# Performance work log

Measured on AMD Instinct MI355X. Metric: run time of the kernel, lower is better.

## Reference

```python
import jax, jax.numpy as jnp
import numpy as np

B, N, NIN, NH, NOUT = 32, 64, 256, 256, 2
E = N * (N - 1)
BN_EPS = 1e-5


def _xavier(k, fan_in, fan_out):
    return jax.random.normal(k, (fan_in, fan_out), jnp.float32) * np.sqrt(2.0 / (fan_in + fan_out))


def _mlp_params(key, n_in, n_hid, n_out):
    k1, k2 = jax.random.split(key)
    return {
        'w1': _xavier(k1, n_in, n_hid), 'b1': jnp.full((n_hid,), 0.1, jnp.float32),
        'w2': _xavier(k2, n_hid, n_out), 'b2': jnp.full((n_out,), 0.1, jnp.float32),
        'g': jnp.ones((n_out,), jnp.float32), 'beta': jnp.zeros((n_out,), jnp.float32),
    }


def setup_inputs() -> dict:
    key = jax.random.key(0)
    ks = jax.random.split(key, 7)
    inputs = jax.random.normal(ks[0], (B, N, NIN), jnp.float32)
    # fully-connected directed graph w/o self loops: edge e = (send i, recv j), i != j
    idx = np.array([(i, j) for i in range(N) for j in range(N) if i != j], dtype=np.int64)
    rel_send = np.zeros((E, N), np.float32)
    rel_rec = np.zeros((E, N), np.float32)
    rel_send[np.arange(E), idx[:, 0]] = 1.0
    rel_rec[np.arange(E), idx[:, 1]] = 1.0
    out = {'inputs': inputs, 'rel_rec': jnp.asarray(rel_rec), 'rel_send': jnp.asarray(rel_send)}
    for name, (ni, nh, no), k in [('mlp1', (NIN, NH, NH), ks[1]),
                                  ('mlp2', (2 * NH, NH, NH), ks[2]),
                                  ('mlp3', (NH, NH, NH), ks[3]),
                                  ('mlp4', (3 * NH, NH, NH), ks[4])]:
        p = _mlp_params(k, ni, nh, no)
        for pk, pv in p.items():
            out[f'{name}_{pk}'] = pv
    out['fc_w'] = _xavier(ks[5], NH, NOUT)
    out['fc_b'] = jnp.full((NOUT,), 0.1, jnp.float32)
    return out


def _mlp(x, w1, b1, w2, b2, g, beta):
    # Linear -> ELU -> Linear -> ELU -> BatchNorm1d (training-mode batch stats, biased var)
    h = jax.nn.elu(x @ w1 + b1)
    h = jax.nn.elu(h @ w2 + b2)
    mean = h.mean(axis=(0, 1))
    var = h.var(axis=(0, 1))
    return (h - mean) * jax.lax.rsqrt(var + BN_EPS) * g + beta


def reference(inputs, rel_rec, rel_send,
              mlp1_w1, mlp1_b1, mlp1_w2, mlp1_b2, mlp1_g, mlp1_beta,
              mlp2_w1, mlp2_b1, mlp2_w2, mlp2_b2, mlp2_g, mlp2_beta,
              mlp3_w1, mlp3_b1, mlp3_w2, mlp3_b2, mlp3_g, mlp3_beta,
              mlp4_w1, mlp4_b1, mlp4_w2, mlp4_b2, mlp4_g, mlp4_beta,
              fc_w, fc_b):
    x = _mlp(inputs, mlp1_w1, mlp1_b1, mlp1_w2, mlp1_b2, mlp1_g, mlp1_beta)  # [B,N,NH]
    # node2edge: gather sender/receiver node features per edge
    s = jnp.einsum('en,bnh->beh', rel_send, x)
    r = jnp.einsum('en,bnh->beh', rel_rec, x)
    x = jnp.concatenate([s, r], axis=-1)  # [B,E,2*NH]
    x = _mlp(x, mlp2_w1, mlp2_b1, mlp2_w2, mlp2_b2, mlp2_g, mlp2_beta)
    x_skip = x
    # edge2node: scatter-sum incoming edges per node, normalized by N
    inc = jnp.einsum('en,beh->bnh', rel_rec, x) / N
    x = _mlp(inc, mlp3_w1, mlp3_b1, mlp3_w2, mlp3_b2, mlp3_g, mlp3_beta)
    s = jnp.einsum('en,bnh->beh', rel_send, x)
    r = jnp.einsum('en,bnh->beh', rel_rec, x)
    x = jnp.concatenate([s, r, x_skip], axis=-1)  # [B,E,3*NH]
    x = _mlp(x, mlp4_w1, mlp4_b1, mlp4_w2, mlp4_b2, mlp4_g, mlp4_beta)
    return x @ fc_w + fc_b  # [B,E,NOUT]
```

## Files before the change

kernel.cpp:

```cpp
#include <hip/hip_runtime.h>

typedef __bf16 bf16_t;
typedef __bf16 bf16x8 __attribute__((ext_vector_type(8)));
typedef float  f32x4  __attribute__((ext_vector_type(4)));

#define NB    64
#define EB    4032
#define BATCH 32
#define H     256
#define M_EDGE (BATCH*EB)
#define M_NODE (BATCH*NB)
#define T2    4
#define BN_EPS 1e-5f

__device__ __forceinline__ void load_lds16(const void* g, void* l) {
    __builtin_amdgcn_global_load_lds(
        (const __attribute__((address_space(1))) unsigned int*)g,
        (__attribute__((address_space(3))) unsigned int*)l, 16, 0, 0);
}
__device__ __forceinline__ float elu(float v) { return v > 0.f ? v : __expf(v) - 1.f; }

template<bool AF32>
__global__ __launch_bounds__(256, 3)
void fused_mlp(const void* __restrict__ A0v,
               const bf16_t* __restrict__ W1f, const float* __restrict__ b1,
               const bf16_t* __restrict__ W2f, const float* __restrict__ b2,
               bf16_t* __restrict__ out, float* __restrict__ stats)
{
    const int m0 = blockIdx.x * 64;
    const int tid = threadIdx.x, wave = tid >> 6, lane = tid & 63;
    const int l15 = lane & 15, quad = lane >> 4;
    const int row = tid >> 2;
    const int c0 = (tid & 3) * 64;

    __shared__ bf16_t h1s[64 * 264];
    __shared__ float  sred[512];

    sred[tid] = 0.f; sred[256 + tid] = 0.f;

    if (AF32) {
        const float* af = (const float*)A0v + (size_t)(m0 + row) * 256 + c0;
#pragma unroll
        for (int j = 0; j < 8; ++j) {
            float4 lo = *(const float4*)(af + j * 8);
            float4 hi = *(const float4*)(af + j * 8 + 4);
            bf16x8 v;
            v[0]=(bf16_t)lo.x; v[1]=(bf16_t)lo.y; v[2]=(bf16_t)lo.z; v[3]=(bf16_t)lo.w;
            v[4]=(bf16_t)hi.x; v[5]=(bf16_t)hi.y; v[6]=(bf16_t)hi.z; v[7]=(bf16_t)hi.w;
            *(bf16x8*)&h1s[row * 264 + c0 + j * 8] = v;
        }
    } else {
        const bf16_t* src = (const bf16_t*)A0v + (size_t)(m0 + row) * 256 + c0;
#pragma unroll
        for (int j = 0; j < 8; ++j)
            *(bf16x8*)&h1s[row * 264 + c0 + j * 8] = *(const bf16x8*)(src + j * 8);
    }

    const bf16_t* W1W = W1f + (size_t)wave * 16384;
    const bf16_t* W2W = W2f + (size_t)wave * 16384;

    bf16x8 bcur[4], bnxt[4];
#pragma unroll
    for (int u = 0; u < 4; ++u)
        bcur[u] = *(const bf16x8*)(W1W + u * 512 + lane * 8);
    __syncthreads();

    f32x4 acc[4][4];
#pragma unroll
    for (int a = 0; a < 4; ++a)
#pragma unroll
        for (int u = 0; u < 4; ++u) acc[a][u] = (f32x4){0.f, 0.f, 0.f, 0.f};

#pragma unroll
    for (int ks = 0; ks < 8; ++ks) {
        if (ks < 7) {
#pragma unroll
            for (int u = 0; u < 4; ++u)
                bnxt[u] = *(const bf16x8*)(W1W + (ks + 1) * 2048 + u * 512 + lane * 8);
        }
        bf16x8 afr[4];
#pragma unroll
        for (int a = 0; a < 4; ++a)
            afr[a] = *(const bf16x8*)&h1s[(a * 16 + l15) * 264 + ks * 32 + quad * 8];
#pragma unroll
        for (int a = 0; a < 4; ++a)
#pragma unroll
            for (int u = 0; u < 4; ++u)
                acc[a][u] = __builtin_amdgcn_mfma_f32_16x16x32_bf16(afr[a], bcur[u], acc[a][u], 0, 0, 0);
#pragma unroll
        for (int u = 0; u < 4; ++u) bcur[u] = bnxt[u];
    }

#pragma unroll
    for (int u = 0; u < 4; ++u)
        bcur[u] = *(const bf16x8*)(W2W + u * 512 + lane * 8);
    __syncthreads();

#pragma unroll
    for (int u = 0; u < 4; ++u) {
        int   col = wave * 64 + u * 16 + l15;
        float bv  = b1[col];
#pragma unroll
        for (int a = 0; a < 4; ++a)
#pragma unroll
            for (int r = 0; r < 4; ++r)
                h1s[(a * 16 + quad * 4 + r) * 264 + col] = (bf16_t)elu(acc[a][u][r] + bv);
    }
    __syncthreads();

#pragma unroll
    for (int a = 0; a < 4; ++a)
#pragma unroll
        for (int u = 0; u < 4; ++u) acc[a][u] = (f32x4){0.f, 0.f, 0.f, 0.f};
#pragma unroll
    for (int ks = 0; ks < 8; ++ks) {
        if (ks < 7) {
#pragma unroll
            for (int u = 0; u < 4; ++u)
                bnxt[u] = *(const bf16x8*)(W2W + (ks + 1) * 2048 + u * 512 + lane * 8);
        }
        bf16x8 afr[4];
#pragma unroll
        for (int a = 0; a < 4; ++a)
            afr[a] = *(const bf16x8*)&h1s[(a * 16 + l15) * 264 + ks * 32 + quad * 8];
#pragma unroll
        for (int a = 0; a < 4; ++a)
#pragma unroll
            for (int u = 0; u < 4; ++u)
                acc[a][u] = __builtin_amdgcn_mfma_f32_16x16x32_bf16(afr[a], bcur[u], acc[a][u], 0, 0, 0);
#pragma unroll
        for (int u = 0; u < 4; ++u) bcur[u] = bnxt[u];
    }
    __syncthreads();

#pragma unroll
    for (int u = 0; u < 4; ++u) {
        int   col = wave * 64 + u * 16 + l15;
        float bv  = b2[col];
        float s = 0.f, q = 0.f;
#pragma unroll
        for (int a = 0; a < 4; ++a)
#pragma unroll
            for (int r = 0; r < 4; ++r) {
                float v = elu(acc[a][u][r] + bv);
                h1s[(a * 16 + quad * 4 + r) * 264 + col] = (bf16_t)v;
                s += v; q += v * v;
            }
        s += __shfl_xor(s, 16); s += __shfl_xor(s, 32);
        q += __shfl_xor(q, 16); q += __shfl_xor(q, 32);
        if (quad == 0) { atomicAdd(&sred[col], s); atomicAdd(&sred[256 + col], q); }
    }
    __syncthreads();

#pragma unroll
    for (int p = 0; p < 8; ++p) {
        int idx = p * 256 + tid;
        int r = idx >> 5, ch = idx & 31;
        *(uint4*)&out[(size_t)(m0 + r) * H + ch * 8] = *(const uint4*)&h1s[r * 264 + ch * 8];
    }
    atomicAdd(&stats[tid],     sred[tid]);
    atomicAdd(&stats[H + tid], sred[256 + tid]);
}

__global__ __launch_bounds__(256)
void node_gemm(const bf16_t* __restrict__ A, const float* __restrict__ statsIn,
               const float* __restrict__ g, const float* __restrict__ beta, float Mcnt,
               const bf16_t* __restrict__ Wt, const float* __restrict__ bias,
               float* __restrict__ out)
{
    const int m0 = blockIdx.x * 64;
    const int nb = blockIdx.y * 256;
    const int tid = threadIdx.x, wave = tid >> 6, lane = tid & 63;
    const int l15 = lane & 15, quad = lane >> 4;
    const int row = tid >> 2;
    const int cx8 = (((tid & 3) ^ ((tid >> 3) & 3))) * 8;
    const int sl8 = (tid & 3) * 8;
    const int xq8 = (quad ^ ((l15 >> 1) & 3)) * 8;
    __shared__ bf16_t As[64 * 32];
    __shared__ bf16_t Bs[256 * 32];
    __shared__ float  ss[512];

    {
        float mean = statsIn[tid] / Mcnt;
        float var  = statsIn[256 + tid] / Mcnt - mean * mean;
        float scl  = g[tid] * rsqrtf(var + BN_EPS);
        ss[tid]       = scl;
        ss[256 + tid] = beta[tid] - mean * scl;
    }
    __syncthreads();

    f32x4 acc[4][4];
#pragma unroll
    for (int t = 0; t < 4; ++t)
#pragma unroll
        for (int u = 0; u < 4; ++u) acc[t][u] = (f32x4){0.f, 0.f, 0.f, 0.f};

    for (int k0 = 0; k0 < 256; k0 += 32) {
        {
            int kc = k0 + cx8;
            bf16x8 v = *(const bf16x8*)(A + (size_t)(m0 + row) * 256 + kc);
            bf16x8 w;
#pragma unroll
            for (int j = 0; j < 8; ++j)
                w[j] = (bf16_t)((float)v[j] * ss[kc + j] + ss[256 + kc + j]);
            *(bf16x8*)&As[row * 32 + sl8] = w;
        }
#pragma unroll
        for (int p = 0; p < 4; ++p)
            load_lds16(Wt + (size_t)(nb + p * 64 + row) * 256 + k0 + cx8,
                       Bs + (p * 256 + wave * 64) * 8);
        __syncthreads();
        bf16x8 afr[4], bfr[4];
#pragma unroll
        for (int t = 0; t < 4; ++t)
            afr[t] = *(const bf16x8*)&As[(t * 16 + l15) * 32 + xq8];
#pragma unroll
        for (int u = 0; u < 4; ++u)
            bfr[u] = *(const bf16x8*)&Bs[(wave * 64 + u * 16 + l15) * 32 + xq8];
#pragma unroll
        for (int t = 0; t < 4; ++t)
#pragma unroll
            for (int u = 0; u < 4; ++u)
                acc[t][u] = __builtin_amdgcn_mfma_f32_16x16x32_bf16(afr[t], bfr[u], acc[t][u], 0, 0, 0);
        __syncthreads();
    }
#pragma unroll
    for (int u = 0; u < 4; ++u) {
        int col = nb + wave * 64 + u * 16 + l15;
        float bv = bias[col];
#pragma unroll
        for (int t = 0; t < 4; ++t)
#pragma unroll
            for (int r = 0; r < 4; ++r)
                out[(size_t)(m0 + t * 16 + quad * 4 + r) * 512 + col] = acc[t][u][r] + bv;
    }
}

__global__ __launch_bounds__(256, 2)
void m2_kernel(const float* __restrict__ PQ, const bf16_t* __restrict__ W2t,
               const float* __restrict__ b2, bf16_t* __restrict__ out,
               float* __restrict__ stats)
{
    const int tile0 = blockIdx.x * T2;
    const int tid = threadIdx.x, wave = tid >> 6, lane = tid & 63;
    const int l15 = lane & 15, quad = lane >> 4;

    __shared__ bf16_t Abuf[2][64 * 264];
    __shared__ float  sred[512];

    bf16x8 Breg[32];
#pragma unroll
    for (int ks = 0; ks < 8; ++ks)
#pragma unroll
        for (int u = 0; u < 4; ++u) {
            int col = wave * 64 + u * 16 + l15;
            Breg[ks * 4 + u] = *(const bf16x8*)(W2t + (size_t)col * 256 + ks * 32 + quad * 8);
        }
    sred[tid] = 0.f; sred[256 + tid] = 0.f;

    auto computeA = [&](int t, int b) {
        int row = tid >> 2;
        int m = (tile0 + t) * 64 + row;
        int bb = m / EB, e = m - bb * EB;
        int sn = e / (NB - 1), rr = e - sn * (NB - 1);
        int rc = rr + (rr >= sn ? 1 : 0);
        const float* Prow = PQ + (size_t)(bb * NB + sn) * 512;
        const float* Qrow = PQ + (size_t)(bb * NB + rc) * 512 + 256;
        int c0 = (tid & 3) * 64;
#pragma unroll
        for (int j = 0; j < 8; ++j) {
            int c = c0 + j * 8;
            float4 p0 = *(const float4*)(Prow + c);
            float4 p1 = *(const float4*)(Prow + c + 4);
            float4 q0 = *(const float4*)(Qrow + c);
            float4 q1 = *(const float4*)(Qrow + c + 4);
            bf16x8 v;
            v[0]=(bf16_t)elu(p0.x+q0.x); v[1]=(bf16_t)elu(p0.y+q0.y);
            v[2]=(bf16_t)elu(p0.z+q0.z); v[3]=(bf16_t)elu(p0.w+q0.w);
            v[4]=(bf16_t)elu(p1.x+q1.x); v[5]=(bf16_t)elu(p1.y+q1.y);
            v[6]=(bf16_t)elu(p1.z+q1.z); v[7]=(bf16_t)elu(p1.w+q1.w);
            *(bf16x8*)&Abuf[b][row * 264 + c] = v;
        }
    };

    computeA(0, 0);
    __syncthreads();

    for (int t = 0; t < T2; ++t) {
        const int cur = t & 1, nxt = cur ^ 1;
        if (t + 1 < T2) computeA(t + 1, nxt);

        f32x4 acc[4][4];
#pragma unroll
        for (int a = 0; a < 4; ++a)
#pragma unroll
            for (int u = 0; u < 4; ++u) acc[a][u] = (f32x4){0.f, 0.f, 0.f, 0.f};
#pragma unroll
        for (int ks = 0; ks < 8; ++ks) {
            bf16x8 afr[4];
#pragma unroll
            for (int a = 0; a < 4; ++a)
                afr[a] = *(const bf16x8*)&Abuf[cur][(a * 16 + l15) * 264 + ks * 32 + quad * 8];
#pragma unroll
            for (int a = 0; a < 4; ++a)
#pragma unroll
                for (int u = 0; u < 4; ++u)
                    acc[a][u] = __builtin_amdgcn_mfma_f32_16x16x32_bf16(afr[a], Breg[ks * 4 + u], acc[a][u], 0, 0, 0);
        }
        __syncthreads();

#pragma unroll
        for (int u = 0; u < 4; ++u) {
            int   col = wave * 64 + u * 16 + l15;
            float bv  = b2[col];
            float s = 0.f, q = 0.f;
#pragma unroll
            for (int a = 0; a < 4; ++a)
#pragma unroll
                for (int r = 0; r < 4; ++r) {
                    float v = elu(acc[a][u][r] + bv);
                    Abuf[cur][(a * 16 + quad * 4 + r) * 264 + col] = (bf16_t)v;
                    s += v; q += v * v;
                }
            s += __shfl_xor(s, 16); s += __shfl_xor(s, 32);
            q += __shfl_xor(q, 16); q += __shfl_xor(q, 32);
            if (quad == 0) { atomicAdd(&sred[col], s); atomicAdd(&sred[256 + col], q); }
        }
        __syncthreads();

        size_t m0 = (size_t)(tile0 + t) * 64;
#pragma unroll
        for (int p = 0; p < 8; ++p) {
            int idx = p * 256 + tid;
            int r = idx >> 5, ch = idx & 31;
            *(uint4*)&out[(m0 + r) * H + ch * 8] = *(const uint4*)&Abuf[cur][r * 264 + ch * 8];
        }
        __syncthreads();
    }
    atomicAdd(&stats[tid],     sred[tid]);
    atomicAdd(&stats[H + tid], sred[256 + tid]);
}

__global__ __launch_bounds__(256, 3)
void m4_kernel(const bf16_t* __restrict__ h2, const bf16_t* __restrict__ Wskf,
               const float* __restrict__ RS, const bf16_t* __restrict__ W4f,
               const float* __restrict__ b2, bf16_t* __restrict__ out,
               float* __restrict__ stats)
{
    const int m0 = blockIdx.x * 64;
    const int tid = threadIdx.x, wave = tid >> 6, lane = tid & 63;
    const int l15 = lane & 15, quad = lane >> 4;
    const int row = tid >> 2;
    const int cx8 = (((tid & 3) ^ ((tid >> 3) & 3))) * 8;
    const int xq8 = (quad ^ ((l15 >> 1) & 3)) * 8;

    __shared__ bf16_t h1s[8 * 2048];
    __shared__ float  sred[512];

    sred[tid] = 0.f; sred[256 + tid] = 0.f;

    const int bb  = m0 / EB;
    const int e0  = m0 - bb * EB;
    const int sn0 = e0 / (NB - 1);
    const int rr0 = e0 - sn0 * (NB - 1);
    const float* RSb = RS + (size_t)(bb * NB) * 512;

#pragma unroll
    for (int ks = 0; ks < 8; ++ks)
        load_lds16(h2 + (size_t)(m0 + row) * 256 + ks * 32 + cx8,
                   h1s + ks * 2048 + wave * 512);

    f32x4 acc[4][4];
#pragma unroll
    for (int a = 0; a < 4; ++a)
#pragma unroll
        for (int r = 0; r < 4; ++r) {
            int ro = a * 16 + quad * 4 + r;
            int t  = rr0 + ro;
            int wrap = (t >= NB - 1) ? 1 : 0;
            int sn = sn0 + wrap;
            int rr = t - (wrap ? (NB - 1) : 0);
            int rc = rr + (rr >= sn ? 1 : 0);
            const float* Srow = RSb + (size_t)sn * 512;
            const float* Rrow = RSb + (size_t)rc * 512 + 256;
#pragma unroll
            for (int u = 0; u < 4; ++u) {
                int co = wave * 64 + u * 16 + l15;
                acc[a][u][r] = Srow[co] + Rrow[co];
            }
        }

    const bf16_t* WskW = Wskf + (size_t)wave * 16384;
    const bf16_t* W4W  = W4f  + (size_t)wave * 16384;

    bf16x8 bcur[4], bnxt[4];
#pragma unroll
    for (int u = 0; u < 4; ++u)
        bcur[u] = *(const bf16x8*)(WskW + u * 512 + lane * 8);
    __syncthreads();

#pragma unroll
    for (int ks = 0; ks < 8; ++ks) {
        if (ks < 7) {
#pragma unroll
            for (int u = 0; u < 4; ++u)
                bnxt[u] = *(const bf16x8*)(WskW + (ks + 1) * 2048 + u * 512 + lane * 8);
        }
        bf16x8 afr[4];
#pragma unroll
        for (int a = 0; a < 4; ++a)
            afr[a] = *(const bf16x8*)&h1s[ks * 2048 + (a * 16 + l15) * 32 + xq8];
#pragma unroll
        for (int a = 0; a < 4; ++a)
#pragma unroll
            for (int u = 0; u < 4; ++u)
                acc[a][u] = __builtin_amdgcn_mfma_f32_16x16x32_bf16(afr[a], bcur[u], acc[a][u], 0, 0, 0);
#pragma unroll
        for (int u = 0; u < 4; ++u) bcur[u] = bnxt[u];
    }

#pragma unroll
    for (int u = 0; u < 4; ++u)
        bcur[u] = *(const bf16x8*)(W4W + u * 512 + lane * 8);
    __syncthreads();

#pragma unroll
    for (int u = 0; u < 4; ++u) {
        const int ks = wave * 2 + (u >> 1);
        const int qw = (u & 1) * 2 + (l15 >> 3);
        const int j  = l15 & 7;
#pragma unroll
        for (int a = 0; a < 4; ++a)
#pragma unroll
            for (int r = 0; r < 4; ++r) {
                int rw = a * 16 + quad * 4 + r;
                int qp = qw ^ ((rw >> 1) & 3);
                h1s[ks * 2048 + rw * 32 + qp * 8 + j] = (bf16_t)elu(acc[a][u][r]);
            }
    }
    __syncthreads();

#pragma unroll
    for (int a = 0; a < 4; ++a)
#pragma unroll
        for (int u = 0; u < 4; ++u) acc[a][u] = (f32x4){0.f, 0.f, 0.f, 0.f};
#pragma unroll
    for (int ks = 0; ks < 8; ++ks) {
        if (ks < 7) {
#pragma unroll
            for (int u = 0; u < 4; ++u)
                bnxt[u] = *(const bf16x8*)(W4W + (ks + 1) * 2048 + u * 512 + lane * 8);
        }
        bf16x8 afr[4];
#pragma unroll
        for (int a = 0; a < 4; ++a)
            afr[a] = *(const bf16x8*)&h1s[ks * 2048 + (a * 16 + l15) * 32 + xq8];
#pragma unroll
        for (int a = 0; a < 4; ++a)
#pragma unroll
            for (int u = 0; u < 4; ++u)
                acc[a][u] = __builtin_amdgcn_mfma_f32_16x16x32_bf16(afr[a], bcur[u], acc[a][u], 0, 0, 0);
#pragma unroll
        for (int u = 0; u < 4; ++u) bcur[u] = bnxt[u];
    }
    __syncthreads();

#pragma unroll
    for (int u = 0; u < 4; ++u) {
        const int col = wave * 64 + u * 16 + l15;
        const float bv = b2[col];
        const int ks = wave * 2 + (u >> 1);
        const int qw = (u & 1) * 2 + (l15 >> 3);
        const int j  = l15 & 7;
        float s = 0.f, q = 0.f;
#pragma unroll
        for (int a = 0; a < 4; ++a)
#pragma unroll
            for (int r = 0; r < 4; ++r) {
                float v = elu(acc[a][u][r] + bv);
                int rw = a * 16 + quad * 4 + r;
                int qp = qw ^ ((rw >> 1) & 3);
                h1s[ks * 2048 + rw * 32 + qp * 8 + j] = (bf16_t)v;
                s += v; q += v * v;
            }
        s += __shfl_xor(s, 16); s += __shfl_xor(s, 32);
        q += __shfl_xor(q, 16); q += __shfl_xor(q, 32);
        if (quad == 0) { atomicAdd(&sred[col], s); atomicAdd(&sred[256 + col], q); }
    }
    __syncthreads();

#pragma unroll
    for (int p = 0; p < 8; ++p) {
        int idx = p * 256 + tid;
        int r = idx >> 5, ch = idx & 31;
        *(uint4*)&out[(size_t)(m0 + r) * H + ch * 8] =
            *(const uint4*)&h1s[(ch >> 2) * 2048 + r * 32 + (((ch & 3) ^ ((r >> 1) & 3)) * 8)];
    }
    atomicAdd(&stats[tid],     sred[tid]);
    atomicAdd(&stats[H + tid], sred[256 + tid]);
}

__global__ void prep(const float* __restrict__ w1a, bf16_t* __restrict__ wt1a,
                     const float* __restrict__ w1b, bf16_t* __restrict__ wt1b,
                     const float* __restrict__ w2b, bf16_t* __restrict__ wt2b,
                     const float* __restrict__ w3a, bf16_t* __restrict__ wt3a,
                     const float* __restrict__ w3b, bf16_t* __restrict__ wt3b,
                     const float* __restrict__ w4b, bf16_t* __restrict__ wt4b,
                     const float* __restrict__ w2a, bf16_t* __restrict__ wtpq,
                     const float* __restrict__ w4a, bf16_t* __restrict__ wtrs,
                     const float* __restrict__ b2a, float* __restrict__ biasPQ,
                     float* __restrict__ stats)
{
    int blk = blockIdx.x, tid = threadIdx.x;
    if (blk < 1536) {
        int grp = blk >> 8, lb = blk & 255;
        int idx = lb * 256 + tid;
        int k = idx >> 8, n = idx & 255;
        if (grp == 2) {
            wt2b[n * 256 + k] = (bf16_t)w2b[idx];
        } else {
            const float* w; bf16_t* wt;
            switch (grp) {
                case 0: w = w1a; wt = wt1a; break;
                case 1: w = w1b; wt = wt1b; break;
                case 3: w = w3a; wt = wt3a; break;
                case 4: w = w3b; wt = wt3b; break;
                default: w = w4b; wt = wt4b; break;
            }
            int wv = n >> 6, u = (n >> 4) & 3, l15 = n & 15;
            int ks = k >> 5, qd = (k >> 3) & 3, j = k & 7;
            wt[wv * 16384 + ks * 2048 + u * 512 + (qd * 16 + l15) * 8 + j] = (bf16_t)w[idx];
        }
    } else if (blk < 2560) {
        int lb = blk - 1536;
        const float* w = (lb < 512) ? w2a : w4a;
        bf16_t* wt = (lb < 512) ? wtpq : wtrs;
        int c = lb & 511, k = tid;
        float v = (c < 256) ? w[k * 256 + c] : w[(256 + k) * 256 + (c - 256)];
        wt[c * 256 + k] = (bf16_t)v;
    } else if (blk == 2560) {
        biasPQ[tid] = b2a[tid];
        biasPQ[256 + tid] = 0.f;
    } else {
        for (int j = 0; j < 8; ++j) stats[j * 256 + tid] = 0.f;
    }
}

__global__ void prep2(const float* __restrict__ w4a, const float* __restrict__ stats2,
                      const float* __restrict__ g2, const float* __restrict__ be2,
                      const float* __restrict__ b4a, bf16_t* __restrict__ wt,
                      float* __restrict__ bias)
{
    __shared__ float sh2s[256];
    int blk = blockIdx.x, tid = threadIdx.x;
    float mean = stats2[tid] / (float)M_EDGE;
    float var  = stats2[256 + tid] / (float)M_EDGE - mean * mean;
    float scl  = g2[tid] * rsqrtf(var + BN_EPS);
    if (blk < 256) {
        int n = blk, k = tid;
        int wv = n >> 6, u = (n >> 4) & 3, l15 = n & 15;
        int ks = k >> 5, qd = (k >> 3) & 3, j = k & 7;
        wt[wv * 16384 + ks * 2048 + u * 512 + (qd * 16 + l15) * 8 + j] =
            (bf16_t)(w4a[(512 + tid) * 256 + blk] * scl);
    } else {
        sh2s[tid] = be2[tid] - mean * scl;
        __syncthreads();
        float acc = 0.f;
        for (int k = 0; k < 256; ++k)
            acc += sh2s[k] * w4a[(512 + k) * 256 + tid];
        bias[tid] = b4a[tid] + acc;
        bias[256 + tid] = 0.f;
    }
}

__global__ void edge2node(const bf16_t* __restrict__ x2, const float* __restrict__ stats2,
                          const float* __restrict__ g2, const float* __restrict__ be2,
                          bf16_t* __restrict__ inc)
{
    int bn = blockIdx.x, bb = bn >> 6, n = bn & 63;
    int g = threadIdx.x >> 5, t = threadIdx.x & 31;
    __shared__ float part[8][256];
    __shared__ float ss[512];
    {
        int c = threadIdx.x;
        float mean = stats2[c] / (float)M_EDGE;
        float var  = stats2[256 + c] / (float)M_EDGE - mean * mean;
        float scl  = g2[c] * rsqrtf(var + BN_EPS);
        ss[c]       = scl;
        ss[256 + c] = be2[c] - mean * scl;
    }
    const bf16_t* base = x2 + (size_t)bb * EB * H;
    float a[8] = {0.f,0.f,0.f,0.f,0.f,0.f,0.f,0.f};
    for (int i = g; i < NB; i += 8) {
        if (i == n) continue;
        int e = i * (NB - 1) + n - (n > i ? 1 : 0);
        bf16x8 v = *(const bf16x8*)&base[(size_t)e * H + t * 8];
#pragma unroll
        for (int j = 0; j < 8; ++j) a[j] += (float)v[j];
    }
#pragma unroll
    for (int j = 0; j < 8; ++j) part[g][t * 8 + j] = a[j];
    __syncthreads();
    int c = threadIdx.x;
    float s = 0.f;
#pragma unroll
    for (int g2i = 0; g2i < 8; ++g2i) s += part[g2i][c];
    inc[(size_t)bn * H + c] = (bf16_t)(s * (1.f / 64.f) * ss[c] + ss[256 + c] * (63.f / 64.f));
}

__global__ void fc_kernel(const bf16_t* __restrict__ x4, const float* __restrict__ stats4,
                          const float* __restrict__ g4, const float* __restrict__ be4,
                          const float* __restrict__ fcw, const float* __restrict__ fcb,
                          float* __restrict__ out)
{
    __shared__ float ss[512];
    {
        int c = threadIdx.x;
        float mean = stats4[c] / (float)M_EDGE;
        float var  = stats4[256 + c] / (float)M_EDGE - mean * mean;
        float scl  = g4[c] * rsqrtf(var + BN_EPS);
        ss[c]       = scl;
        ss[256 + c] = be4[c] - mean * scl;
    }
    __syncthreads();
    int row  = blockIdx.x * 8 + (threadIdx.x >> 5);
    int t    = threadIdx.x & 31;
    bf16x8 v8 = *(const bf16x8*)(x4 + (size_t)row * H + t * 8);
    float s0 = 0.f, s1 = 0.f;
#pragma unroll
    for (int j = 0; j < 8; ++j) {
        int c = t * 8 + j;
        float v = (float)v8[j] * ss[c] + ss[256 + c];
        s0 += v * fcw[c * 2];
        s1 += v * fcw[c * 2 + 1];
    }
#pragma unroll
    for (int off = 16; off; off >>= 1) {
        s0 += __shfl_down(s0, off, 32);
        s1 += __shfl_down(s1, off, 32);
    }
    if (t == 0) {
        out[(size_t)row * 2]     = s0 + fcb[0];
        out[(size_t)row * 2 + 1] = s1 + fcb[1];
    }
}

extern "C" void kernel_launch(void* const* d_in, const int* in_sizes, int n_in,
                              void* d_out, int out_size, void* d_ws, size_t ws_size,
                              hipStream_t stream)
{
    (void)in_sizes; (void)n_in; (void)out_size; (void)ws_size;
    const float* inp = (const float*)d_in[0];
    const float* w1a = (const float*)d_in[3];  const float* b1a = (const float*)d_in[4];
    const float* w1b = (const float*)d_in[5];  const float* b1b = (const float*)d_in[6];
    const float* g1  = (const float*)d_in[7];  const float* be1 = (const float*)d_in[8];
    const float* w2a = (const float*)d_in[9];  const float* b2a = (const float*)d_in[10];
    const float* w2b = (const float*)d_in[11]; const float* b2b = (const float*)d_in[12];
    const float* g2  = (const float*)d_in[13]; const float* be2 = (const float*)d_in[14];
    const float* w3a = (const float*)d_in[15]; const float* b3a = (const float*)d_in[16];
    const float* w3b = (const float*)d_in[17]; const float* b3b = (const float*)d_in[18];
    const float* g3  = (const float*)d_in[19]; const float* be3 = (const float*)d_in[20];
    const float* w4a = (const float*)d_in[21]; const float* b4a = (const float*)d_in[22];
    const float* w4b = (const float*)d_in[23]; const float* b4b = (const float*)d_in[24];
    const float* g4  = (const float*)d_in[25]; const float* be4 = (const float*)d_in[26];
    const float* fcw = (const float*)d_in[27]; const float* fcb = (const float*)d_in[28];

    char* p = (char*)d_ws;
    auto alloc = [&](size_t nbytes) { char* r = p; p += (nbytes + 255) & ~(size_t)255; return r; };

    bf16_t* wt1a = (bf16_t*)alloc(256 * 256 * 2);
    bf16_t* wt1b = (bf16_t*)alloc(256 * 256 * 2);
    bf16_t* wt2b = (bf16_t*)alloc(256 * 256 * 2);
    bf16_t* wt3a = (bf16_t*)alloc(256 * 256 * 2);
    bf16_t* wt3b = (bf16_t*)alloc(256 * 256 * 2);
    bf16_t* wt4b = (bf16_t*)alloc(256 * 256 * 2);
    bf16_t* wtpq = (bf16_t*)alloc(512 * 256 * 2);
    bf16_t* wtrs = (bf16_t*)alloc(512 * 256 * 2);
    bf16_t* wtsk = (bf16_t*)alloc(256 * 256 * 2);
    float*  biasPQ = (float*)alloc(512 * sizeof(float));
    float*  biasRS = (float*)alloc(512 * sizeof(float));
    float*  stats  = (float*)alloc(4 * 512 * sizeof(float));
    bf16_t* x1   = (bf16_t*)alloc((size_t)M_NODE * H * 2);
    bf16_t* incb = (bf16_t*)alloc((size_t)M_NODE * H * 2);
    bf16_t* x3   = (bf16_t*)alloc((size_t)M_NODE * H * 2);
    float*  PQ   = (float*)alloc((size_t)M_NODE * 512 * sizeof(float));
    float*  RS   = (float*)alloc((size_t)M_NODE * 512 * sizeof(float));
    bf16_t* h2   = (bf16_t*)alloc((size_t)M_EDGE * H * 2);
    bf16_t* h4   = (bf16_t*)alloc((size_t)M_EDGE * H * 2);

    prep<<<2562, 256, 0, stream>>>(w1a, wt1a, w1b, wt1b, w2b, wt2b, w3a, wt3a,
                                   w3b, wt3b, w4b, wt4b, w2a, wtpq, w4a, wtrs,
                                   b2a, biasPQ, stats);

    fused_mlp<true ><<<M_NODE / 64, 256, 0, stream>>>(inp, wt1a, b1a, wt1b, b1b, x1, stats + 0);

    { dim3 g(M_NODE / 64, 2);
      node_gemm<<<g, 256, 0, stream>>>(x1, stats + 0, g1, be1, (float)M_NODE, wtpq, biasPQ, PQ); }

    m2_kernel<<<M_EDGE / (64 * T2), 256, 0, stream>>>(PQ, wt2b, b2b, h2, stats + 512);

    edge2node<<<M_NODE, 256, 0, stream>>>(h2, stats + 512, g2, be2, incb);
    fused_mlp<false><<<M_NODE / 64, 256, 0, stream>>>(incb, wt3a, b3a, wt3b, b3b, x3, stats + 1024);

    prep2<<<257, 256, 0, stream>>>(w4a, stats + 512, g2, be2, b4a, wtsk, biasRS);
    { dim3 g(M_NODE / 64, 2);
      node_gemm<<<g, 256, 0, stream>>>(x3, stats + 1024, g3, be3, (float)M_NODE, wtrs, biasRS, RS); }

    m4_kernel<<<M_EDGE / 64, 256, 0, stream>>>(h2, wtsk, RS, wt4b, b4b, h4, stats + 1536);

    fc_kernel<<<M_EDGE / 8, 256, 0, stream>>>(h4, stats + 1536, g4, be4, fcw, fcb, (float*)d_out);
}
```

Baseline: 352.5 us.

## Restructure m2 kernel to one tile per block with swizzled LDS and streamed weights

The edge-layer second GEMM kernel no longer loops over four 64-row tiles with the whole W2 slice held in registers and a double-buffered A tile. Each block now handles a single 64-row tile. It builds the ELU(P+Q) tile into an XOR-swizzled LDS layout and streams pre-swizzled W2 fragments from global memory per k-step, the same way m4_kernel does. The prep kernel now emits W2 in that fragment layout. This cuts register pressure (occupancy 2 to 3 blocks per CU) and LDS bank conflicts, at the cost of reloading weights per tile and losing the overlap of A computation with the MFMAs.

```diff
diff --git a/kernel.cpp b/kernel.cpp
--- a/kernel.cpp
+++ b/kernel.cpp
@@ -10,7 +10,6 @@
 #define H     256
 #define M_EDGE (BATCH*EB)
 #define M_NODE (BATCH*NB)
-#define T2    4
 #define BN_EPS 1e-5f
 
 __device__ __forceinline__ void load_lds16(const void* g, void* l) {
@@ -236,37 +235,37 @@
     }
 }
 
-__global__ __launch_bounds__(256, 2)
-void m2_kernel(const float* __restrict__ PQ, const bf16_t* __restrict__ W2t,
+__global__ __launch_bounds__(256, 3)
+void m2_kernel(const float* __restrict__ PQ, const bf16_t* __restrict__ W2f,
                const float* __restrict__ b2, bf16_t* __restrict__ out,
                float* __restrict__ stats)
 {
-    const int tile0 = blockIdx.x * T2;
+    const int m0 = blockIdx.x * 64;
     const int tid = threadIdx.x, wave = tid >> 6, lane = tid & 63;
     const int l15 = lane & 15, quad = lane >> 4;
-
-    __shared__ bf16_t Abuf[2][64 * 264];
+    const int row = tid >> 2;
+    const int c0 = (tid & 3) * 64;
+    const int xq8 = (quad ^ ((l15 >> 1) & 3)) * 8;
+
+    __shared__ bf16_t h1s[8 * 2048];
     __shared__ float  sred[512];
 
-    bf16x8 Breg[32];
-#pragma unroll
-    for (int ks = 0; ks < 8; ++ks)
-#pragma unroll
-        for (int u = 0; u < 4; ++u) {
-            int col = wave * 64 + u * 16 + l15;
-            Breg[ks * 4 + u] = *(const bf16x8*)(W2t + (size_t)col * 256 + ks * 32 + quad * 8);
-        }
     sred[tid] = 0.f; sred[256 + tid] = 0.f;
 
-    auto computeA = [&](int t, int b) {
-        int row = tid >> 2;
-        int m = (tile0 + t) * 64 + row;
-        int bb = m / EB, e = m - bb * EB;
-        int sn = e / (NB - 1), rr = e - sn * (NB - 1);
+    const int bb  = m0 / EB;
+    const int e0  = m0 - bb * EB;
+    const int sn0 = e0 / (NB - 1);
+    const int rr0 = e0 - sn0 * (NB - 1);
+
+    {
+        int t  = rr0 + row;
+        int wrap = (t >= NB - 1) ? 1 : 0;
+        int sn = sn0 + wrap;
+        int rr = t - (wrap ? (NB - 1) : 0);
         int rc = rr + (rr >= sn ? 1 : 0);
         const float* Prow = PQ + (size_t)(bb * NB + sn) * 512;
         const float* Qrow = PQ + (size_t)(bb * NB + rc) * 512 + 256;
-        int c0 = (tid & 3) * 64;
+        const int rs = ((row >> 1) & 3);
 #pragma unroll
         for (int j = 0; j < 8; ++j) {
             int c = c0 + j * 8;
@@ -279,177 +278,29 @@
             v[2]=(bf16_t)elu(p0.z+q0.z); v[3]=(bf16_t)elu(p0.w+q0.w);
             v[4]=(bf16_t)elu(p1.x+q1.x); v[5]=(bf16_t)elu(p1.y+q1.y);
             v[6]=(bf16_t)elu(p1.z+q1.z); v[7]=(bf16_t)elu(p1.w+q1.w);
-            *(bf16x8*)&Abuf[b][row * 264 + c] = v;
-        }
-    };
-
-    computeA(0, 0);
-    __syncthreads();
-
-    for (int t = 0; t < T2; ++t) {
-        const int cur = t & 1, nxt = cur ^ 1;
-        if (t + 1 < T2) computeA(t + 1, nxt);
-
-        f32x4 acc[4][4];
-#pragma unroll
-        for (int a = 0; a < 4; ++a)
-#pragma unroll
-            for (int u = 0; u < 4; ++u) acc[a][u] = (f32x4){0.f, 0.f, 0.f, 0.f};
-#pragma unroll
-        for (int ks = 0; ks < 8; ++ks) {
-            bf16x8 afr[4];
-#pragma unroll
-            for (int a = 0; a < 4; ++a)
-                afr[a] = *(const bf16x8*)&Abuf[cur][(a * 16 + l15) * 264 + ks * 32 + quad * 8];
-#pragma unroll
-            for (int a = 0; a < 4; ++a)
-#pragma unroll
-                for (int u = 0; u < 4; ++u)
-                    acc[a][u] = __builtin_amdgcn_mfma_f32_16x16x32_bf16(afr[a], Breg[ks * 4 + u], acc[a][u], 0, 0, 0);
-        }
-        __syncthreads();
-
-#pragma unroll
-        for (int u = 0; u < 4; ++u) {
-            int   col = wave * 64 + u * 16 + l15;
-            float bv  = b2[col];
-            float s = 0.f, q = 0.f;
-#pragma unroll
-            for (int a = 0; a < 4; ++a)
-#pragma unroll
-                for (int r = 0; r < 4; ++r) {
-                    float v = elu(acc[a][u][r] + bv);
-                    Abuf[cur][(a * 16 + quad * 4 + r) * 264 + col] = (bf16_t)v;
-                    s += v; q += v * v;
-                }
-            s += __shfl_xor(s, 16); s += __shfl_xor(s, 32);
-            q += __shfl_xor(q, 16); q += __shfl_xor(q, 32);
-            if (quad == 0) { atomicAdd(&sred[col], s); atomicAdd(&sred[256 + col], q); }
-        }
-        __syncthreads();
-
-        size_t m0 = (size_t)(tile0 + t) * 64;
-#pragma unroll
-        for (int p = 0; p < 8; ++p) {
-            int idx = p * 256 + tid;
-            int r = idx >> 5, ch = idx & 31;
-            *(uint4*)&out[(m0 + r) * H + ch * 8] = *(const uint4*)&Abuf[cur][r * 264 + ch * 8];
-        }
-        __syncthreads();
-    }
-    atomicAdd(&stats[tid],     sred[tid]);
-    atomicAdd(&stats[H + tid], sred[256 + tid]);
-}
-
-__global__ __launch_bounds__(256, 3)
-void m4_kernel(const bf16_t* __restrict__ h2, const bf16_t* __restrict__ Wskf,
-               const float* __restrict__ RS, const bf16_t* __restrict__ W4f,
-               const float* __restrict__ b2, bf16_t* __restrict__ out,
-               float* __restrict__ stats)
-{
-    const int m0 = blockIdx.x * 64;
-    const int tid = threadIdx.x, wave = tid >> 6, lane = tid & 63;
-    const int l15 = lane & 15, quad = lane >> 4;
-    const int row = tid >> 2;
-    const int cx8 = (((tid & 3) ^ ((tid >> 3) & 3))) * 8;
-    const int xq8 = (quad ^ ((l15 >> 1) & 3)) * 8;
-
-    __shared__ bf16_t h1s[8 * 2048];
-    __shared__ float  sred[512];
-
-    sred[tid] = 0.f; sred[256 + tid] = 0.f;
-
-    const int bb  = m0 / EB;
-    const int e0  = m0 - bb * EB;
-    const int sn0 = e0 / (NB - 1);
-    const int rr0 = e0 - sn0 * (NB - 1);
-    const float* RSb = RS + (size_t)(bb * NB) * 512;
-
-#pragma unroll
-    for (int ks = 0; ks < 8; ++ks)
-        load_lds16(h2 + (size_t)(m0 + row) * 256 + ks * 32 + cx8,
-                   h1s + ks * 2048 + wave * 512);
+            *(bf16x8*)&h1s[(c >> 5) * 2048 + row * 32 + ((((c >> 3) & 3) ^ rs) * 8)] = v;
+        }
+    }
+
+    const bf16_t* W2W = W2f + (size_t)wave * 16384;
+    bf16x8 bcur[4], bnxt[4];
+#pragma unroll
+    for (int u = 0; u < 4; ++u)
+        bcur[u] = *(const bf16x8*)(W2W + u * 512 + lane * 8);
+    __syncthreads();
 
     f32x4 acc[4][4];
 #pragma unroll
     for (int a = 0; a < 4; ++a)
 #pragma unroll
-        for (int r = 0; r < 4; ++r) {
-            int ro = a * 16 + quad * 4 + r;
-            int t  = rr0 + ro;
-            int wrap = (t >= NB - 1) ? 1 : 0;
-            int sn = sn0 + wrap;
-            int rr = t - (wrap ? (NB - 1) : 0);
-            int rc = rr + (rr >= sn ? 1 : 0);
-            const float* Srow = RSb + (size_t)sn * 512;
-            const float* Rrow = RSb + (size_t)rc * 512 + 256;
-#pragma unroll
-            for (int u = 0; u < 4; ++u) {
-                int co = wave * 64 + u * 16 + l15;
-                acc[a][u][r] = Srow[co] + Rrow[co];
-            }
-        }
-
-    const bf16_t* WskW = Wskf + (size_t)wave * 16384;
-    const bf16_t* W4W  = W4f  + (size_t)wave * 16384;
-
-    bf16x8 bcur[4], bnxt[4];
-#pragma unroll
-    for (int u = 0; u < 4; ++u)
-        bcur[u] = *(const bf16x8*)(WskW + u * 512 + lane * 8);
-    __syncthreads();
+        for (int u = 0; u < 4; ++u) acc[a][u] = (f32x4){0.f, 0.f, 0.f, 0.f};
 
 #pragma unroll
     for (int ks = 0; ks < 8; ++ks) {
         if (ks < 7) {
 #pragma unroll
             for (int u = 0; u < 4; ++u)
-                bnxt[u] = *(const bf16x8*)(WskW + (ks + 1) * 2048 + u * 512 + lane * 8);
-        }
-        bf16x8 afr[4];
-#pragma unroll
-        for (int a = 0; a < 4; ++a)
-            afr[a] = *(const bf16x8*)&h1s[ks * 2048 + (a * 16 + l15) * 32 + xq8];
-#pragma unroll
-        for (int a = 0; a < 4; ++a)
-#pragma unroll
-            for (int u = 0; u < 4; ++u)
-                acc[a][u] = __builtin_amdgcn_mfma_f32_16x16x32_bf16(afr[a], bcur[u], acc[a][u], 0, 0, 0);
-#pragma unroll
-        for (int u = 0; u < 4; ++u) bcur[u] = bnxt[u];
-    }
-
-#pragma unroll
-    for (int u = 0; u < 4; ++u)
-        bcur[u] = *(const bf16x8*)(W4W + u * 512 + lane * 8);
-    __syncthreads();
-
-#pragma unroll
-    for (int u = 0; u < 4; ++u) {
-        const int ks = wave * 2 + (u >> 1);
-        const int qw = (u & 1) * 2 + (l15 >> 3);
-        const int j  = l15 & 7;
-#pragma unroll
-        for (int a = 0; a < 4; ++a)
-#pragma unroll
-            for (int r = 0; r < 4; ++r) {
-                int rw = a * 16 + quad * 4 + r;
-                int qp = qw ^ ((rw >> 1) & 3);
-                h1s[ks * 2048 + rw * 32 + qp * 8 + j] = (bf16_t)elu(acc[a][u][r]);
-            }
-    }
-    __syncthreads();
-
-#pragma unroll
-    for (int a = 0; a < 4; ++a)
-#pragma unroll
-        for (int u = 0; u < 4; ++u) acc[a][u] = (f32x4){0.f, 0.f, 0.f, 0.f};
-#pragma unroll
-    for (int ks = 0; ks < 8; ++ks) {
-        if (ks < 7) {
-#pragma unroll
-            for (int u = 0; u < 4; ++u)
-                bnxt[u] = *(const bf16x8*)(W4W + (ks + 1) * 2048 + u * 512 + lane * 8);
+                bnxt[u] = *(const bf16x8*)(W2W + (ks + 1) * 2048 + u * 512 + lane * 8);
         }
         bf16x8 afr[4];
 #pragma unroll
@@ -500,6 +351,165 @@
     atomicAdd(&stats[H + tid], sred[256 + tid]);
 }
 
+__global__ __launch_bounds__(256, 3)
+void m4_kernel(const bf16_t* __restrict__ h2, const bf16_t* __restrict__ Wskf,
+               const float* __restrict__ RS, const bf16_t* __restrict__ W4f,
+               const float* __restrict__ b2, bf16_t* __restrict__ out,
+               float* __restrict__ stats)
+{
+    const int m0 = blockIdx.x * 64;
+    const int tid = threadIdx.x, wave = tid >> 6, lane = tid & 63;
+    const int l15 = lane & 15, quad = lane >> 4;
+    const int row = tid >> 2;
+    const int cx8 = (((tid & 3) ^ ((tid >> 3) & 3))) * 8;
+    const int xq8 = (quad ^ ((l15 >> 1) & 3)) * 8;
+
+    __shared__ bf16_t h1s[8 * 2048];
+    __shared__ float  sred[512];
+
+    sred[tid] = 0.f; sred[256 + tid] = 0.f;
+
+    const int bb  = m0 / EB;
+    const int e0  = m0 - bb * EB;
+    const int sn0 = e0 / (NB - 1);
+    const int rr0 = e0 - sn0 * (NB - 1);
+    const float* RSb = RS + (size_t)(bb * NB) * 512;
+
+#pragma unroll
+    for (int ks = 0; ks < 8; ++ks)
+        load_lds16(h2 + (size_t)(m0 + row) * 256 + ks * 32 + cx8,
+                   h1s + ks * 2048 + wave * 512);
+
+    f32x4 acc[4][4];
+#pragma unroll
+    for (int a = 0; a < 4; ++a)
+#pragma unroll
+        for (int r = 0; r < 4; ++r) {
+            int ro = a * 16 + quad * 4 + r;
+            int t  = rr0 + ro;
+            int wrap = (t >= NB - 1) ? 1 : 0;
+            int sn = sn0 + wrap;
+            int rr = t - (wrap ? (NB - 1) : 0);
+            int rc = rr + (rr >= sn ? 1 : 0);
+            const float* Srow = RSb + (size_t)sn * 512;
+            const float* Rrow = RSb + (size_t)rc * 512 + 256;
+#pragma unroll
+            for (int u = 0; u < 4; ++u) {
+                int co = wave * 64 + u * 16 + l15;
+                acc[a][u][r] = Srow[co] + Rrow[co];
+            }
+        }
+
+    const bf16_t* WskW = Wskf + (size_t)wave * 16384;
+    const bf16_t* W4W  = W4f  + (size_t)wave * 16384;
+
+    bf16x8 bcur[4], bnxt[4];
+#pragma unroll
+    for (int u = 0; u < 4; ++u)
+        bcur[u] = *(const bf16x8*)(WskW + u * 512 + lane * 8);
+    __syncthreads();
+
+#pragma unroll
+    for (int ks = 0; ks < 8; ++ks) {
+        if (ks < 7) {
+#pragma unroll
+            for (int u = 0; u < 4; ++u)
+                bnxt[u] = *(const bf16x8*)(WskW + (ks + 1) * 2048 + u * 512 + lane * 8);
+        }
+        bf16x8 afr[4];
+#pragma unroll
+        for (int a = 0; a < 4; ++a)
+            afr[a] = *(const bf16x8*)&h1s[ks * 2048 + (a * 16 + l15) * 32 + xq8];
+#pragma unroll
+        for (int a = 0; a < 4; ++a)
+#pragma unroll
+            for (int u = 0; u < 4; ++u)
+                acc[a][u] = __builtin_amdgcn_mfma_f32_16x16x32_bf16(afr[a], bcur[u], acc[a][u], 0, 0, 0);
+#pragma unroll
+        for (int u = 0; u < 4; ++u) bcur[u] = bnxt[u];
+    }
+
+#pragma unroll
+    for (int u = 0; u < 4; ++u)
+        bcur[u] = *(const bf16x8*)(W4W + u * 512 + lane * 8);
+    __syncthreads();
+
+#pragma unroll
+    for (int u = 0; u < 4; ++u) {
+        const int ks = wave * 2 + (u >> 1);
+        const int qw = (u & 1) * 2 + (l15 >> 3);
+        const int j  = l15 & 7;
+#pragma unroll
+        for (int a = 0; a < 4; ++a)
+#pragma unroll
+            for (int r = 0; r < 4; ++r) {
+                int rw = a * 16 + quad * 4 + r;
+                int qp = qw ^ ((rw >> 1) & 3);
+                h1s[ks * 2048 + rw * 32 + qp * 8 + j] = (bf16_t)elu(acc[a][u][r]);
+            }
+    }
+    __syncthreads();
+
+#pragma unroll
+    for (int a = 0; a < 4; ++a)
+#pragma unroll
+        for (int u = 0; u < 4; ++u) acc[a][u] = (f32x4){0.f, 0.f, 0.f, 0.f};
+#pragma unroll
+    for (int ks = 0; ks < 8; ++ks) {
+        if (ks < 7) {
+#pragma unroll
+            for (int u = 0; u < 4; ++u)
+                bnxt[u] = *(const bf16x8*)(W4W + (ks + 1) * 2048 + u * 512 + lane * 8);
+        }
+        bf16x8 afr[4];
+#pragma unroll
+        for (int a = 0; a < 4; ++a)
+            afr[a] = *(const bf16x8*)&h1s[ks * 2048 + (a * 16 + l15) * 32 + xq8];
+#pragma unroll
+        for (int a = 0; a < 4; ++a)
+#pragma unroll
+            for (int u = 0; u < 4; ++u)
+                acc[a][u] = __builtin_amdgcn_mfma_f32_16x16x32_bf16(afr[a], bcur[u], acc[a][u], 0, 0, 0);
+#pragma unroll
+        for (int u = 0; u < 4; ++u) bcur[u] = bnxt[u];
+    }
+    __syncthreads();
+
+#pragma unroll
+    for (int u = 0; u < 4; ++u) {
+        const int col = wave * 64 + u * 16 + l15;
+        const float bv = b2[col];
+        const int ks = wave * 2 + (u >> 1);
+        const int qw = (u & 1) * 2 + (l15 >> 3);
+        const int j  = l15 & 7;
+        float s = 0.f, q = 0.f;
+#pragma unroll
+        for (int a = 0; a < 4; ++a)
+#pragma unroll
+            for (int r = 0; r < 4; ++r) {
+                float v = elu(acc[a][u][r] + bv);
+                int rw = a * 16 + quad * 4 + r;
+                int qp = qw ^ ((rw >> 1) & 3);
+                h1s[ks * 2048 + rw * 32 + qp * 8 + j] = (bf16_t)v;
+                s += v; q += v * v;
+            }
+        s += __shfl_xor(s, 16); s += __shfl_xor(s, 32);
+        q += __shfl_xor(q, 16); q += __shfl_xor(q, 32);
+        if (quad == 0) { atomicAdd(&sred[col], s); atomicAdd(&sred[256 + col], q); }
+    }
+    __syncthreads();
+
+#pragma unroll
+    for (int p = 0; p < 8; ++p) {
+        int idx = p * 256 + tid;
+        int r = idx >> 5, ch = idx & 31;
+        *(uint4*)&out[(size_t)(m0 + r) * H + ch * 8] =
+            *(const uint4*)&h1s[(ch >> 2) * 2048 + r * 32 + (((ch & 3) ^ ((r >> 1) & 3)) * 8)];
+    }
+    atomicAdd(&stats[tid],     sred[tid]);
+    atomicAdd(&stats[H + tid], sred[256 + tid]);
+}
+
 __global__ void prep(const float* __restrict__ w1a, bf16_t* __restrict__ wt1a,
                      const float* __restrict__ w1b, bf16_t* __restrict__ wt1b,
                      const float* __restrict__ w2b, bf16_t* __restrict__ wt2b,
@@ -516,21 +526,18 @@
         int grp = blk >> 8, lb = blk & 255;
         int idx = lb * 256 + tid;
         int k = idx >> 8, n = idx & 255;
-        if (grp == 2) {
-            wt2b[n * 256 + k] = (bf16_t)w2b[idx];
-        } else {
-            const float* w; bf16_t* wt;
-            switch (grp) {
-                case 0: w = w1a; wt = wt1a; break;
-                case 1: w = w1b; wt = wt1b; break;
-                case 3: w = w3a; wt = wt3a; break;
-                case 4: w = w3b; wt = wt3b; break;
-                default: w = w4b; wt = wt4b; break;
-            }
-            int wv = n >> 6, u = (n >> 4) & 3, l15 = n & 15;
-            int ks = k >> 5, qd = (k >> 3) & 3, j = k & 7;
-            wt[wv * 16384 + ks * 2048 + u * 512 + (qd * 16 + l15) * 8 + j] = (bf16_t)w[idx];
-        }
+        const float* w; bf16_t* wt;
+        switch (grp) {
+            case 0: w = w1a; wt = wt1a; break;
+            case 1: w = w1b; wt = wt1b; break;
+            case 2: w = w2b; wt = wt2b; break;
+            case 3: w = w3a; wt = wt3a; break;
+            case 4: w = w3b; wt = wt3b; break;
+            default: w = w4b; wt = wt4b; break;
+        }
+        int wv = n >> 6, u = (n >> 4) & 3, l15 = n & 15;
+        int ks = k >> 5, qd = (k >> 3) & 3, j = k & 7;
+        wt[wv * 16384 + ks * 2048 + u * 512 + (qd * 16 + l15) * 8 + j] = (bf16_t)w[idx];
     } else if (blk < 2560) {
         int lb = blk - 1536;
         const float* w = (lb < 512) ? w2a : w4a;
@@ -697,7 +704,7 @@
     { dim3 g(M_NODE / 64, 2);
       node_gemm<<<g, 256, 0, stream>>>(x1, stats + 0, g1, be1, (float)M_NODE, wtpq, biasPQ, PQ); }
 
-    m2_kernel<<<M_EDGE / (64 * T2), 256, 0, stream>>>(PQ, wt2b, b2b, h2, stats + 512);
+    m2_kernel<<<M_EDGE / 64, 256, 0, stream>>>(PQ, wt2b, b2b, h2, stats + 512);
 
     edge2node<<<M_NODE, 256, 0, stream>>>(h2, stats + 512, g2, be2, incb);
     fused_mlp<false><<<M_NODE / 64, 256, 0, stream>>>(incb, wt3a, b3a, wt3b, b3b, x3, stats + 1024);
```

Result: no change. 352.8 us (+0.1%).
